# Optimization experiments

Measured on AMD Instinct MI355X. Metric: run time of the kernel, lower is better.

## Reference

```python
import jax, jax.numpy as jnp
import numpy as np

R_MAX = 5.0
AVG_NEIGH = 16.0
F = 64          # hidden scalar channels (hidden_irreps count of 0e)
NB = 8          # num_bessel
LMAX = 2
S = 9           # (LMAX+1)^2 spherical-harmonic components
NE = 10         # num_elements
G = 4           # num_graphs
T = 2           # num_interactions
L_OF_LM = np.array([0, 1, 1, 1, 2, 2, 2, 2, 2])


def spherical_harmonics(u):
    # real SH up to l=2, e3nn 'component' normalization; u: [E,3] unit vectors
    x, y, z = u[:, 0], u[:, 1], u[:, 2]
    s3, s5, s15 = 3.0 ** 0.5, 5.0 ** 0.5, 15.0 ** 0.5
    return jnp.stack([
        jnp.ones_like(x),
        s3 * x, s3 * y, s3 * z,
        s15 * x * y, s15 * y * z, (s5 / 2.0) * (3.0 * z * z - 1.0),
        s15 * x * z, (s15 / 2.0) * (x * x - y * y),
    ], axis=-1)  # [E, 9]


def radial_embedding(r):
    # Bessel basis * polynomial cutoff (p=5), as in MACE RadialEmbeddingBlock
    r_safe = jnp.maximum(r, 1e-6)
    n = jnp.arange(1, NB + 1, dtype=r.dtype)  # [NB]
    bessel = jnp.sqrt(2.0 / R_MAX) * jnp.sin(n[None, :] * jnp.pi * r_safe[:, None] / R_MAX) / r_safe[:, None]
    u = r / R_MAX
    p = 5.0
    f = (1.0 - 0.5 * (p + 1) * (p + 2) * u ** 5 + p * (p + 2) * u ** 6 - 0.5 * p * (p + 1) * u ** 7)
    f = f * (u < 1.0)
    return bessel * f[:, None]  # [E, NB]


def setup_inputs() -> dict:
    key = jax.random.key(0)
    ks = jax.random.split(key, 24)
    N, E = 20000, 320000
    positions = jax.random.normal(ks[0], (N, 3), dtype=jnp.float32) * 5.0
    species = jax.random.randint(ks[1], (N,), 0, NE)
    node_attrs = jax.nn.one_hot(species, NE, dtype=jnp.float32)
    edge_index = jax.random.randint(ks[2], (2, E), 0, N)
    shifts = jnp.zeros((E, 3), dtype=jnp.float32)
    batch = jnp.sort(jax.random.randint(ks[3], (N,), 0, G)).astype(jnp.int32)
    charges = jax.random.normal(ks[4], (N,), dtype=jnp.float32) * 0.1
    sc = 1.0 / np.sqrt(F)
    params = {
        'atomic_energies': jax.random.normal(ks[5], (NE,), dtype=jnp.float32),
        'W_embed': jax.random.normal(ks[6], (NE, F), dtype=jnp.float32),
        'Wr0': jax.random.normal(ks[7], (T, NB, 64), dtype=jnp.float32) / np.sqrt(NB),
        'Wr1': jax.random.normal(ks[8], (T, 64, 64), dtype=jnp.float32) / 8.0,
        'Wr2': jax.random.normal(ks[9], (T, 64, F * (LMAX + 1)), dtype=jnp.float32) / 8.0,
        'Wmix': jax.random.normal(ks[10], (T, LMAX + 1, F, F), dtype=jnp.float32) * sc,
        'Wprod': jax.random.normal(ks[11], (T, NE, F, 3), dtype=jnp.float32) * sc,
        'Wread0': jax.random.normal(ks[12], (F,), dtype=jnp.float32) * sc,
        'Wm1': jax.random.normal(ks[13], (F, 16), dtype=jnp.float32) * sc,
        'wm2': jax.random.normal(ks[14], (16,), dtype=jnp.float32) * 0.25,
        'Wq': jax.random.normal(ks[15], (T, F), dtype=jnp.float32) * sc,
    }
    return dict(positions=positions, node_attrs=node_attrs, shifts=shifts,
                charges=charges, edge_index=edge_index, batch=batch, **params)


def _forward(positions, node_attrs, shifts, charges,
             atomic_energies, W_embed, Wr0, Wr1, Wr2, Wmix, Wprod,
             Wread0, Wm1, wm2, Wq, edge_index, batch):
    N = positions.shape[0]
    src, dst = edge_index[0], edge_index[1]
    # isolated-atom reference energies
    node_e0 = node_attrs @ atomic_energies                       # [N]
    e0 = jax.ops.segment_sum(node_e0, batch, num_segments=G)     # [G]
    # edge geometry
    vec = positions[dst] - positions[src] + shifts               # [E,3]
    lengths = jnp.linalg.norm(vec, axis=-1)                      # [E]
    len_safe = jnp.where(lengths > 1e-6, lengths, 1.0)
    unit = vec / len_safe[:, None]
    edge_attrs = spherical_harmonics(unit)                       # [E,S]
    edge_feats = radial_embedding(lengths)                       # [E,NB]
    # node embedding: scalars only, rest of irreps zero
    node_feats = jnp.zeros((N, F, S), dtype=positions.dtype)
    node_feats = node_feats.at[:, :, 0].set(node_attrs @ W_embed)
    charge_density = charges[:, None] * jnp.ones((1, 1), positions.dtype)  # [N,1] formal charges (l=0)
    lm = jnp.asarray(L_OF_LM)
    energy = e0
    for t in range(T):
        # radial MLP -> per-edge tensor-product weights [E,F,LMAX+1]
        h = jax.nn.silu(edge_feats @ Wr0[t])
        h = jax.nn.silu(h @ Wr1[t])
        w = (h @ Wr2[t]).reshape(-1, F, LMAX + 1)
        wl = w[:, :, lm]                                         # [E,F,S]
        s_src = node_feats[src, :, 0]                            # [E,F] gather
        msg = wl * s_src[:, :, None] * edge_attrs[:, None, :]    # [E,F,S]
        A = jax.ops.segment_sum(msg, dst, num_segments=N) / AVG_NEIGH  # [N,F,S] scatter
        # per-l linear channel mixing
        A = jnp.einsum('nfs,sfg->ngs', A, Wmix[t][lm])
        # symmetric product basis (correlation 3), element-dependent weights
        wp = jnp.einsum('ne,efc->nfc', node_attrs, Wprod[t])     # [N,F,3]
        p1 = A[:, :, 0]                                          # scalar invariant
        p2 = jnp.sum(A * A, axis=-1)                             # norm invariant
        scale = wp[:, :, 0] + wp[:, :, 1] * p1 + wp[:, :, 2] * p2
        new_feats = A * scale[:, :, None]
        if t > 0:
            new_feats = new_feats + node_feats                   # residual self-connection
        node_feats = new_feats
        scal = node_feats[:, :, 0]
        if t == T - 1:
            node_en = jax.nn.silu(scal @ Wm1) @ wm2              # nonlinear readout
        else:
            node_en = scal @ Wread0                              # linear readout
        energy = energy + jax.ops.segment_sum(node_en, batch, num_segments=G)
        charge_density = charge_density + (scal @ Wq[t])[:, None]
    return energy  # [G]


def reference(positions, node_attrs, shifts, charges, edge_index, batch,
              atomic_energies, W_embed, Wr0, Wr1, Wr2, Wmix, Wprod,
              Wread0, Wm1, wm2, Wq):
    return _forward(positions, node_attrs, shifts, charges,
                    atomic_energies, W_embed, Wr0, Wr1, Wr2, Wmix, Wprod,
                    Wread0, Wm1, wm2, Wq, edge_index, batch)
```

## Files before the change

kernel.cpp:

```cpp
#include <hip/hip_runtime.h>
#include <hip/hip_bf16.h>

#define F 64
#define NB 8
#define NE 10
#define GSEG 4
#define EPW 256
#define NTAB 2048

typedef __attribute__((ext_vector_type(8))) short short8v;
typedef __attribute__((ext_vector_type(4))) float float4v;

__device__ __forceinline__ float silu(float x) {
    return x / (1.0f + __expf(-x));
}

__device__ __forceinline__ float bcast(float v, int lane) {
    return __uint_as_float(__builtin_amdgcn_readlane(__float_as_uint(v), lane));
}

__device__ __forceinline__ unsigned short f2bf(float x) {
    unsigned int u = __float_as_uint(x);
    u += 0x7FFFu + ((u >> 16) & 1u);
    return (unsigned short)(u >> 16);
}

__global__ __launch_bounds__(256) void init_and_tables(
    const float* __restrict__ node_attrs, const float* __restrict__ AE,
    const float* __restrict__ W_embed, const int* __restrict__ batch,
    const float* __restrict__ pos,
    float* __restrict__ S0, float* __restrict__ epart,
    int* __restrict__ deg, float4* __restrict__ pos4,
    int* __restrict__ spec, int N, int nodeBlocks,
    const float* __restrict__ Wr0, const float* __restrict__ Wr1,
    const float* __restrict__ Wr2, float* __restrict__ Tab,
    const float* __restrict__ Wmix, unsigned short* __restrict__ Wbt,
    int tabBlocks)
{
    int w = threadIdx.x >> 6, lane = threadIdx.x & 63;

    if (blockIdx.x < (unsigned)nodeBlocks) {
        int n = blockIdx.x * 4 + w;
        if (n >= N) return;
        float sc = 0.0f, e0 = 0.0f;
        int sp = 0;
        #pragma unroll
        for (int e = 0; e < NE; e++) {
            float a = node_attrs[n * NE + e];
            sc = fmaf(a, W_embed[e * F + lane], sc);
            e0 = fmaf(a, AE[e], e0);
            if (a > 0.5f) sp = e;
        }
        S0[(size_t)n * F + lane] = sc;
        if (lane == 0) {
            deg[n] = 0;
            spec[n] = sp;
            pos4[n] = make_float4(pos[n * 3], pos[n * 3 + 1], pos[n * 3 + 2], 0.f);
            atomicAdd(&epart[batch[n] * EPW + (n & (EPW - 1))], e0);
        }
        return;
    }

    if (blockIdx.x >= (unsigned)(nodeBlocks + tabBlocks)) {
        int i = (blockIdx.x - nodeBlocks - tabBlocks) * 256 + threadIdx.x;
        if (i >= 2 * 3 * 4096) return;
        int tl = i >> 12;
        int gf = i & 4095;
        int g = gf >> 6, f = gf & 63;
        Wbt[i] = f2bf(Wmix[(size_t)(tl * 64 + f) * 64 + g] * 0.0625f);
        return;
    }

    const int blocksPerTab = (NTAB + 1 + 3) / 4;
    int bid = blockIdx.x - nodeBlocks;
    int tab = bid / blocksPerTab;
    int eidx = (bid - tab * blocksPerTab) * 4 + w;
    if (eidx > NTAB) return;
    const float* W0 = Wr0 + tab * 512;
    const float* W1 = Wr1 + tab * 4096;
    const float* W2 = Wr2 + tab * 12288;

    float r = (float)eidx * (5.0f / NTAB);
    float rs = fmaxf(r, 1e-6f);
    float s1, c1;
    __sincosf(0.6283185307179586f * rs, &s1, &c1);
    float u = r * 0.2f;
    float u2 = u * u, u4 = u2 * u2, u5 = u4 * u, u6 = u5 * u, u7 = u6 * u;
    float fc = 1.0f - 21.0f * u5 + 35.0f * u6 - 15.0f * u7;
    float pref = 0.6324555320336759f / rs * fc;
    float ef[NB];
    {
        float sp = 0.0f, sc_ = s1, tc = 2.0f * c1;
        #pragma unroll
        for (int k = 0; k < NB; k++) {
            ef[k] = pref * sc_;
            float sn = tc * sc_ - sp;
            sp = sc_; sc_ = sn;
        }
    }

    float a1 = 0.0f;
    #pragma unroll
    for (int k = 0; k < NB; k++) a1 = fmaf(ef[k], W0[k * 64 + lane], a1);
    float h1 = silu(a1);

    float a2 = 0.0f;
    #pragma unroll 8
    for (int k = 0; k < 64; k++)
        a2 = fmaf(bcast(h1, k), W1[k * 64 + lane], a2);
    float h2 = silu(a2);

    float w0 = 0.f, w1 = 0.f, w2 = 0.f;
    #pragma unroll 8
    for (int k = 0; k < 64; k++) {
        float hk = bcast(h2, k);
        const float* wr = W2 + k * 192 + lane * 3;
        w0 = fmaf(hk, wr[0], w0);
        w1 = fmaf(hk, wr[1], w1);
        w2 = fmaf(hk, wr[2], w2);
    }

    float* Trow = Tab + ((size_t)tab * (NTAB + 1) + eidx) * 192;
    Trow[lane] = w0;
    Trow[64 + lane] = w1;
    Trow[128 + lane] = w2;
}

__global__ __launch_bounds__(256) void edge_prep(
    const float4* __restrict__ pos4, const float* __restrict__ shifts,
    const int* __restrict__ EI, int E,
    float4* __restrict__ geoFull, int* __restrict__ deg)
{
    int e = blockIdx.x * 256 + threadIdx.x;
    if (e >= E) return;
    int s = EI[e], d = EI[E + e];
    float4 pd = pos4[d], ps = pos4[s];
    float vx = pd.x - ps.x + shifts[e * 3 + 0];
    float vy = pd.y - ps.y + shifts[e * 3 + 1];
    float vz = pd.z - ps.z + shifts[e * 3 + 2];
    float len = sqrtf(vx * vx + vy * vy + vz * vz);
    float ls = (len > 1e-6f) ? len : 1.0f;
    float inv = 1.0f / ls;
    geoFull[e] = make_float4(vx * inv, vy * inv, vz * inv, len);
    if (len < 5.0f) atomicAdd(&deg[d], 1);
}

__global__ __launch_bounds__(256) void alloc_start(
    const int* __restrict__ deg, int* __restrict__ start,
    int* __restrict__ cursor, int* __restrict__ total, int N)
{
    __shared__ int wsum[4];
    __shared__ int gbase;
    int t = threadIdx.x;
    int n = blockIdx.x * 256 + t;
    int lane = t & 63, w = t >> 6;
    int v = (n < N) ? deg[n] : 0;
    int inc = v;
    #pragma unroll
    for (int off = 1; off < 64; off <<= 1) {
        int u = __shfl_up(inc, off);
        if (lane >= off) inc += u;
    }
    if (lane == 63) wsum[w] = inc;
    __syncthreads();
    if (t == 0) {
        int s0 = wsum[0], s1 = wsum[1], s2 = wsum[2], s3 = wsum[3];
        int bs = s0 + s1 + s2 + s3;
        wsum[0] = 0; wsum[1] = s0; wsum[2] = s0 + s1; wsum[3] = s0 + s1 + s2;
        gbase = atomicAdd(total, bs);
    }
    __syncthreads();
    if (n < N) {
        int st = gbase + wsum[w] + (inc - v);
        start[n] = st;
        cursor[n] = st;
    }
}

__global__ __launch_bounds__(256) void csr_fill(
    const float4* __restrict__ geoFull, const int* __restrict__ EI, int E,
    int* __restrict__ cursor,
    float4* __restrict__ geoS, int* __restrict__ srcS, int EB)
{
    int e = blockIdx.x * 256 + threadIdx.x;
    if (e >= E) return;
    float4 gv = geoFull[e];
    if (gv.w < 5.0f) {
        int d = EI[E + e];
        int p = atomicAdd(&cursor[d], 1);
        if (p < EB) {
            geoS[p] = gv;
            srcS[p] = EI[e];
        }
    }
}

template <int PHASE>
__global__ __launch_bounds__(512) void gather_mix(
    const float4* __restrict__ geoS, const int* __restrict__ srcS,
    const float* __restrict__ Tab,
    const int* __restrict__ start, const int* __restrict__ deg,
    const unsigned short* __restrict__ Wbt,
    const float* __restrict__ Wprodt, const int* __restrict__ spec,
    const int* __restrict__ batch,
    const float* __restrict__ Wread0, const float* __restrict__ Wm1,
    const float* __restrict__ wm2,
    const float* __restrict__ Sin, float* __restrict__ Sout,
    float* __restrict__ epart, int N)
{
    __shared__ float Osh[9 * 1088];

    int t = threadIdx.x;
    int lane = t & 63, w = t >> 6;
    int l15 = lane & 15, quad = lane >> 4;
    int n0 = blockIdx.x * 16;

    int nn[2] = {n0 + w, n0 + w + 8};
    int b[2] = {0, 0}, sp[2] = {0, 0};
    float resid[2] = {0.f, 0.f};
    #pragma unroll
    for (int j = 0; j < 2; j++) {
        if (nn[j] < N) {
            b[j] = batch[nn[j]];
            sp[j] = spec[nn[j]];
            if (PHASE == 1) resid[j] = Sin[(size_t)nn[j] * F + lane];
        }
    }

    const float s3 = 1.7320508075688772f;
    const float s5h = 1.1180339887498948f;
    const float s15 = 3.8729833462074170f;
    const float s15h = 1.9364916731037085f;
    #pragma unroll
    for (int j = 0; j < 2; j++) {
        int n = nn[j];
        int v = w + j * 8;
        float am[9] = {0.f, 0.f, 0.f, 0.f, 0.f, 0.f, 0.f, 0.f, 0.f};
        if (n < N) {
            int st = start[n], iend = st + deg[n];
            for (int i = st; i < iend; i++) {
                float4 gv = geoS[i];
                int srcn = srcS[i];
                float sv = Sin[(size_t)srcn * F + lane];
                float scaled = gv.w * (NTAB / 5.0f);
                int idx = (int)scaled;
                float fr = scaled - (float)idx;
                const float* T0 = Tab + (size_t)idx * 192;
                float wa = T0[lane],       wb = T0[192 + lane];
                float wc = T0[64 + lane],  wd = T0[256 + lane];
                float we = T0[128 + lane], wf_ = T0[320 + lane];
                float w0 = fmaf(fr, wb - wa, wa);
                float w1 = fmaf(fr, wd - wc, wc);
                float w2 = fmaf(fr, wf_ - we, we);
                float ux = gv.x, uy = gv.y, uz = gv.z;
                float m0 = w0 * sv, m1 = w1 * sv, m2 = w2 * sv;
                am[0] += m0;
                am[1] = fmaf(m1, s3 * ux, am[1]);
                am[2] = fmaf(m1, s3 * uy, am[2]);
                am[3] = fmaf(m1, s3 * uz, am[3]);
                am[4] = fmaf(m2, s15 * ux * uy, am[4]);
                am[5] = fmaf(m2, s15 * uy * uz, am[5]);
                am[6] = fmaf(m2, s5h * (3.0f * uz * uz - 1.0f), am[6]);
                am[7] = fmaf(m2, s15 * ux * uz, am[7]);
                am[8] = fmaf(m2, s15h * (ux * ux - uy * uy), am[8]);
            }
        }
        #pragma unroll
        for (int s = 0; s < 9; s++)
            ((unsigned short*)(Osh + s * 1088))[v * 68 + lane] = f2bf(am[s]);
    }

    float wp[2][3] = {{0.f, 0.f, 0.f}, {0.f, 0.f, 0.f}};
    #pragma unroll
    for (int j = 0; j < 2; j++) {
        if (nn[j] < N) {
            const float* W = Wprodt + (sp[j] * F + lane) * 3;
            wp[j][0] = W[0]; wp[j][1] = W[1]; wp[j][2] = W[2];
        }
    }
    __syncthreads();

    for (int s = w; s < 9; s += 8) {
        int l = (s == 0) ? 0 : ((s < 4) ? 1 : 2);
        const unsigned short* Bp = Wbt + l * 4096 + (size_t)l15 * 64;
        const unsigned short* Ar =
            (const unsigned short*)(Osh + s * 1088) + l15 * 68;
        short8v a0 = *(const short8v*)(Ar + quad * 8);
        short8v a1 = *(const short8v*)(Ar + 32 + quad * 8);
        #pragma unroll
        for (int nt = 0; nt < 4; nt++) {
            short8v b0 = *(const short8v*)(Bp + nt * 1024 + quad * 8);
            short8v b1 = *(const short8v*)(Bp + nt * 1024 + 32 + quad * 8);
            float4v acc = {0.f, 0.f, 0.f, 0.f};
            acc = __builtin_amdgcn_mfma_f32_16x16x32_bf16(a0, b0, acc, 0, 0, 0);
            acc = __builtin_amdgcn_mfma_f32_16x16x32_bf16(a1, b1, acc, 0, 0, 0);
            #pragma unroll
            for (int r = 0; r < 4; r++)
                Osh[s * 1088 + (quad * 4 + r) * 68 + nt * 16 + l15] = acc[r];
        }
    }
    __syncthreads();

    #pragma unroll
    for (int j = 0; j < 2; j++) {
        int n = nn[j];
        if (n >= N) continue;
        int v = w + j * 8;
        float bb[9];
        #pragma unroll
        for (int s = 0; s < 9; s++) bb[s] = Osh[s * 1088 + v * 68 + lane];

        float p1 = bb[0];
        float p2 = 0.f;
        #pragma unroll
        for (int s = 0; s < 9; s++) p2 = fmaf(bb[s], bb[s], p2);
        float scale = wp[j][0] + wp[j][1] * p1 + wp[j][2] * p2;
        float sc0 = bb[0] * scale;

        if (PHASE == 0) {
            Sout[(size_t)n * F + lane] = sc0;
            float vv = sc0 * Wread0[lane];
            #pragma unroll
            for (int off = 32; off > 0; off >>= 1) vv += __shfl_xor(vv, off);
            if (lane == 0) atomicAdd(&epart[b[j] * EPW + (n & (EPW - 1))], vv);
        } else {
            sc0 += resid[j];
            int gi = lane & 15;
            float acc = 0.0f;
            #pragma unroll 8
            for (int k = 0; k < 64; k++)
                acc = fmaf(bcast(sc0, k), Wm1[k * 16 + gi], acc);
            float vv = (lane < 16) ? silu(acc) * wm2[gi] : 0.0f;
            #pragma unroll
            for (int off = 32; off > 0; off >>= 1) vv += __shfl_xor(vv, off);
            if (lane == 0) atomicAdd(&epart[b[j] * EPW + (n & (EPW - 1))], vv);
        }
    }
}

__global__ __launch_bounds__(256) void reduce_energy(
    const float* __restrict__ epart, float* __restrict__ out)
{
    int t = threadIdx.x;
    __shared__ float ps[GSEG][4];
    for (int b = 0; b < GSEG; b++) {
        float v = epart[b * EPW + t];
        #pragma unroll
        for (int off = 32; off > 0; off >>= 1) v += __shfl_xor(v, off);
        if ((t & 63) == 0) ps[b][t >> 6] = v;
    }
    __syncthreads();
    if (t < GSEG) out[t] = ps[t][0] + ps[t][1] + ps[t][2] + ps[t][3];
}

extern "C" void kernel_launch(void* const* d_in, const int* in_sizes, int n_in,
                              void* d_out, int out_size, void* d_ws, size_t ws_size,
                              hipStream_t stream) {
    const float* positions  = (const float*)d_in[0];
    const float* node_attrs = (const float*)d_in[1];
    const float* shifts     = (const float*)d_in[2];
    const int*   edge_index = (const int*)d_in[4];
    const int*   batch      = (const int*)d_in[5];
    const float* AE         = (const float*)d_in[6];
    const float* W_embed    = (const float*)d_in[7];
    const float* Wr0        = (const float*)d_in[8];
    const float* Wr1        = (const float*)d_in[9];
    const float* Wr2        = (const float*)d_in[10];
    const float* Wmix       = (const float*)d_in[11];
    const float* Wprod      = (const float*)d_in[12];
    const float* Wread0     = (const float*)d_in[13];
    const float* Wm1        = (const float*)d_in[14];
    const float* wm2        = (const float*)d_in[15];

    int N = in_sizes[0] / 3;
    int E = in_sizes[4] / 2;
    int EB = E / 8;
    float* out = (float*)d_out;

    char* ws = (char*)d_ws;
    size_t off = 0;
    auto alignup = [](size_t v) { return (v + 255) & ~(size_t)255; };
    float4* geoFull = (float4*)(ws + off); off = alignup(off + (size_t)E * sizeof(float4));
    float4* geoS  = (float4*)(ws + off); off = alignup(off + (size_t)EB * sizeof(float4));
    float4* pos4  = (float4*)(ws + off); off = alignup(off + (size_t)N * sizeof(float4));
    float*  S0    = (float*)(ws + off);  off = alignup(off + (size_t)N * F * sizeof(float));
    float*  S1    = (float*)(ws + off);  off = alignup(off + (size_t)N * F * sizeof(float));
    int*    srcS  = (int*)(ws + off);    off = alignup(off + (size_t)EB * sizeof(int));
    int*    deg   = (int*)(ws + off);    off = alignup(off + (size_t)N * sizeof(int));
    int*    start = (int*)(ws + off);    off = alignup(off + (size_t)N * sizeof(int));
    int*    cursor= (int*)(ws + off);    off = alignup(off + (size_t)N * sizeof(int));
    int*    spec  = (int*)(ws + off);    off = alignup(off + (size_t)N * sizeof(int));
    float*  epart = (float*)(ws + off);
    int*    total = (int*)(ws + off + GSEG * EPW * sizeof(float));
    off = alignup(off + GSEG * EPW * sizeof(float) + 128);
    float*  Tab   = (float*)(ws + off);
    off = alignup(off + (size_t)2 * (NTAB + 1) * 192 * sizeof(float));
    unsigned short* Wbt = (unsigned short*)(ws + off);
    off = alignup(off + (size_t)2 * 3 * 4096 * sizeof(unsigned short));

    hipMemsetAsync(epart, 0, GSEG * EPW * sizeof(float) + 128, stream);

    int nodeBlocks4 = (N + 3) / 4;
    int nodeBlocks256 = (N + 255) / 256;
    int edgeBlocks = (E + 255) / 256;
    int tabBlocks = 2 * ((NTAB + 1 + 3) / 4);
    int wbBlocks = (2 * 3 * 4096 + 255) / 256;
    int gmBlocks = (N + 15) / 16;
    size_t tabStride = (size_t)(NTAB + 1) * 192;

    init_and_tables<<<nodeBlocks4 + tabBlocks + wbBlocks, 256, 0, stream>>>(
        node_attrs, AE, W_embed, batch, positions,
        S0, epart, deg, pos4, spec, N, nodeBlocks4,
        Wr0, Wr1, Wr2, Tab, Wmix, Wbt, tabBlocks);
    edge_prep<<<edgeBlocks, 256, 0, stream>>>(pos4, shifts, edge_index, E,
                                              geoFull, deg);
    alloc_start<<<nodeBlocks256, 256, 0, stream>>>(deg, start, cursor, total, N);
    csr_fill<<<edgeBlocks, 256, 0, stream>>>(geoFull, edge_index, E,
                                             cursor, geoS, srcS, EB);

    gather_mix<0><<<gmBlocks, 512, 0, stream>>>(geoS, srcS, Tab, start, deg,
                                                Wbt, Wprod, spec, batch,
                                                Wread0, Wm1, wm2,
                                                S0, S1, epart, N);
    gather_mix<1><<<gmBlocks, 512, 0, stream>>>(geoS, srcS, Tab + tabStride,
                                                start, deg,
                                                Wbt + 3 * 4096,
                                                Wprod + NE * F * 3, spec, batch,
                                                Wread0, Wm1, wm2,
                                                S1, S1, epart, N);

    reduce_energy<<<1, 256, 0, stream>>>(epart, out);
}
```

Before: 211.5 us.

## Split each block's edge range across waves with LDS atomic accumulation

Instead of each wave walking the CSR edge list of its own two destination nodes, all eight waves now stride over the block's contiguous 16-node edge range. A new per-edge destination array lets each wave add its nine SH-weighted messages into shared-memory accumulators with atomics. The fp32 sums are converted to bf16 in place before the MFMA mixing step. The aim is to balance uneven node degrees across waves, at the cost of nine LDS atomics per edge, an extra zeroing pass and an extra dst array written in csr_fill.

```diff
diff --git a/kernel.cpp b/kernel.cpp
--- a/kernel.cpp
+++ b/kernel.cpp
@@ -180,7 +180,8 @@
 __global__ __launch_bounds__(256) void csr_fill(
     const float4* __restrict__ geoFull, const int* __restrict__ EI, int E,
     int* __restrict__ cursor,
-    float4* __restrict__ geoS, int* __restrict__ srcS, int EB)
+    float4* __restrict__ geoS, int* __restrict__ srcS,
+    int* __restrict__ dstS, int EB)
 {
     int e = blockIdx.x * 256 + threadIdx.x;
     if (e >= E) return;
@@ -191,6 +192,7 @@
         if (p < EB) {
             geoS[p] = gv;
             srcS[p] = EI[e];
+            dstS[p] = d;
         }
     }
 }
@@ -198,7 +200,7 @@
 template <int PHASE>
 __global__ __launch_bounds__(512) void gather_mix(
     const float4* __restrict__ geoS, const int* __restrict__ srcS,
-    const float* __restrict__ Tab,
+    const int* __restrict__ dstS, const float* __restrict__ Tab,
     const int* __restrict__ start, const int* __restrict__ deg,
     const unsigned short* __restrict__ Wbt,
     const float* __restrict__ Wprodt, const int* __restrict__ spec,
@@ -226,50 +228,6 @@
             if (PHASE == 1) resid[j] = Sin[(size_t)nn[j] * F + lane];
         }
     }
-
-    const float s3 = 1.7320508075688772f;
-    const float s5h = 1.1180339887498948f;
-    const float s15 = 3.8729833462074170f;
-    const float s15h = 1.9364916731037085f;
-    #pragma unroll
-    for (int j = 0; j < 2; j++) {
-        int n = nn[j];
-        int v = w + j * 8;
-        float am[9] = {0.f, 0.f, 0.f, 0.f, 0.f, 0.f, 0.f, 0.f, 0.f};
-        if (n < N) {
-            int st = start[n], iend = st + deg[n];
-            for (int i = st; i < iend; i++) {
-                float4 gv = geoS[i];
-                int srcn = srcS[i];
-                float sv = Sin[(size_t)srcn * F + lane];
-                float scaled = gv.w * (NTAB / 5.0f);
-                int idx = (int)scaled;
-                float fr = scaled - (float)idx;
-                const float* T0 = Tab + (size_t)idx * 192;
-                float wa = T0[lane],       wb = T0[192 + lane];
-                float wc = T0[64 + lane],  wd = T0[256 + lane];
-                float we = T0[128 + lane], wf_ = T0[320 + lane];
-                float w0 = fmaf(fr, wb - wa, wa);
-                float w1 = fmaf(fr, wd - wc, wc);
-                float w2 = fmaf(fr, wf_ - we, we);
-                float ux = gv.x, uy = gv.y, uz = gv.z;
-                float m0 = w0 * sv, m1 = w1 * sv, m2 = w2 * sv;
-                am[0] += m0;
-                am[1] = fmaf(m1, s3 * ux, am[1]);
-                am[2] = fmaf(m1, s3 * uy, am[2]);
-                am[3] = fmaf(m1, s3 * uz, am[3]);
-                am[4] = fmaf(m2, s15 * ux * uy, am[4]);
-                am[5] = fmaf(m2, s15 * uy * uz, am[5]);
-                am[6] = fmaf(m2, s5h * (3.0f * uz * uz - 1.0f), am[6]);
-                am[7] = fmaf(m2, s15 * ux * uz, am[7]);
-                am[8] = fmaf(m2, s15h * (ux * ux - uy * uy), am[8]);
-            }
-        }
-        #pragma unroll
-        for (int s = 0; s < 9; s++)
-            ((unsigned short*)(Osh + s * 1088))[v * 68 + lane] = f2bf(am[s]);
-    }
-
     float wp[2][3] = {{0.f, 0.f, 0.f}, {0.f, 0.f, 0.f}};
     #pragma unroll
     for (int j = 0; j < 2; j++) {
@@ -278,13 +236,66 @@
             wp[j][0] = W[0]; wp[j][1] = W[1]; wp[j][2] = W[2];
         }
     }
+
+    for (int i = t; i < 9 * 1088; i += 512) Osh[i] = 0.0f;
+    __syncthreads();
+
+    {
+        int lastN = (n0 + 16 <= N ? n0 + 16 : N) - 1;
+        int tStart = start[n0];
+        int tEnd = start[lastN] + deg[lastN];
+        const float s3 = 1.7320508075688772f;
+        const float s5h = 1.1180339887498948f;
+        const float s15 = 3.8729833462074170f;
+        const float s15h = 1.9364916731037085f;
+        for (int i = tStart + w; i < tEnd; i += 8) {
+            float4 gv = geoS[i];
+            int srcn = srcS[i];
+            int nloc = dstS[i] - n0;
+            float sv = Sin[(size_t)srcn * F + lane];
+            float scaled = gv.w * (NTAB / 5.0f);
+            int idx = (int)scaled;
+            float fr = scaled - (float)idx;
+            const float* T0 = Tab + (size_t)idx * 192;
+            float wa = T0[lane],       wb = T0[192 + lane];
+            float wc = T0[64 + lane],  wd = T0[256 + lane];
+            float we = T0[128 + lane], wf_ = T0[320 + lane];
+            float w0 = fmaf(fr, wb - wa, wa);
+            float w1 = fmaf(fr, wd - wc, wc);
+            float w2 = fmaf(fr, wf_ - we, we);
+            float ux = gv.x, uy = gv.y, uz = gv.z;
+            float m0 = w0 * sv, m1 = w1 * sv, m2 = w2 * sv;
+            int base = nloc * 68 + lane;
+            atomicAdd(&Osh[0 * 1088 + base], m0);
+            atomicAdd(&Osh[1 * 1088 + base], m1 * (s3 * ux));
+            atomicAdd(&Osh[2 * 1088 + base], m1 * (s3 * uy));
+            atomicAdd(&Osh[3 * 1088 + base], m1 * (s3 * uz));
+            atomicAdd(&Osh[4 * 1088 + base], m2 * (s15 * ux * uy));
+            atomicAdd(&Osh[5 * 1088 + base], m2 * (s15 * uy * uz));
+            atomicAdd(&Osh[6 * 1088 + base], m2 * (s5h * (3.0f * uz * uz - 1.0f)));
+            atomicAdd(&Osh[7 * 1088 + base], m2 * (s15 * ux * uz));
+            atomicAdd(&Osh[8 * 1088 + base], m2 * (s15h * (ux * ux - uy * uy)));
+        }
+    }
     __syncthreads();
 
     for (int s = w; s < 9; s += 8) {
+        float* slot = Osh + s * 1088;
+        unsigned short* ab = (unsigned short*)slot;
+        float v0[8];
+        #pragma unroll
+        for (int v = 0; v < 8; v++) v0[v] = slot[v * 68 + lane];
+        #pragma unroll
+        for (int v = 0; v < 8; v++) ab[v * 68 + lane] = f2bf(v0[v]);
+        float v1[8];
+        #pragma unroll
+        for (int v = 0; v < 8; v++) v1[v] = slot[(v + 8) * 68 + lane];
+        #pragma unroll
+        for (int v = 0; v < 8; v++) ab[(v + 8) * 68 + lane] = f2bf(v1[v]);
+
         int l = (s == 0) ? 0 : ((s < 4) ? 1 : 2);
         const unsigned short* Bp = Wbt + l * 4096 + (size_t)l15 * 64;
-        const unsigned short* Ar =
-            (const unsigned short*)(Osh + s * 1088) + l15 * 68;
+        const unsigned short* Ar = ab + l15 * 68;
         short8v a0 = *(const short8v*)(Ar + quad * 8);
         short8v a1 = *(const short8v*)(Ar + 32 + quad * 8);
         #pragma unroll
@@ -296,7 +307,7 @@
             acc = __builtin_amdgcn_mfma_f32_16x16x32_bf16(a1, b1, acc, 0, 0, 0);
             #pragma unroll
             for (int r = 0; r < 4; r++)
-                Osh[s * 1088 + (quad * 4 + r) * 68 + nt * 16 + l15] = acc[r];
+                slot[(quad * 4 + r) * 68 + nt * 16 + l15] = acc[r];
         }
     }
     __syncthreads();
@@ -386,6 +397,7 @@
     float*  S0    = (float*)(ws + off);  off = alignup(off + (size_t)N * F * sizeof(float));
     float*  S1    = (float*)(ws + off);  off = alignup(off + (size_t)N * F * sizeof(float));
     int*    srcS  = (int*)(ws + off);    off = alignup(off + (size_t)EB * sizeof(int));
+    int*    dstS  = (int*)(ws + off);    off = alignup(off + (size_t)EB * sizeof(int));
     int*    deg   = (int*)(ws + off);    off = alignup(off + (size_t)N * sizeof(int));
     int*    start = (int*)(ws + off);    off = alignup(off + (size_t)N * sizeof(int));
     int*    cursor= (int*)(ws + off);    off = alignup(off + (size_t)N * sizeof(int));
@@ -416,13 +428,13 @@
                                               geoFull, deg);
     alloc_start<<<nodeBlocks256, 256, 0, stream>>>(deg, start, cursor, total, N);
     csr_fill<<<edgeBlocks, 256, 0, stream>>>(geoFull, edge_index, E,
-                                             cursor, geoS, srcS, EB);
-
-    gather_mix<0><<<gmBlocks, 512, 0, stream>>>(geoS, srcS, Tab, start, deg,
+                                             cursor, geoS, srcS, dstS, EB);
+
+    gather_mix<0><<<gmBlocks, 512, 0, stream>>>(geoS, srcS, dstS, Tab, start, deg,
                                                 Wbt, Wprod, spec, batch,
                                                 Wread0, Wm1, wm2,
                                                 S0, S1, epart, N);
-    gather_mix<1><<<gmBlocks, 512, 0, stream>>>(geoS, srcS, Tab + tabStride,
+    gather_mix<1><<<gmBlocks, 512, 0, stream>>>(geoS, srcS, dstS, Tab + tabStride,
                                                 start, deg,
                                                 Wbt + 3 * 4096,
                                                 Wprod + NE * F * 3, spec, batch,
```

New measurement: 372.5 us. 76.1% more time.
